# Kernel tuning notes

Hardware: AMD Instinct MI355X
Metric: run time of the kernel (lower is better)

The kernel has to match this reference:

```python
import jax, jax.numpy as jnp
import numpy as np

# Model dims (see init_kwargs)
B, N, N_IN, D = 16, 8192, 4096, 8
DT = 1e-3
TAU_MEM, TAU_ADAPT = 0.02, 0.2
ALPHA = float(np.exp(-DT / TAU_MEM))    # membrane leak decay per step
RHO_A = float(np.exp(-DT / TAU_ADAPT))  # threshold-adaptation decay per step
BETA = 1.8                              # adaptive-threshold strength (ALIF)
TH0 = 1.0                               # base firing threshold
P_SPIKE = 0.05                          # presynaptic firing prob for inputs


def setup_inputs() -> dict:
    key = jax.random.key(0)
    k = jax.random.split(key, 6)
    V = jax.random.normal(k[0], (B, N), jnp.float32)          # membrane potentials
    a = jax.random.uniform(k[1], (B, N), dtype=jnp.float32)   # ALIF adaptation state
    # Delayed-spike ring buffer [D, B, N] and external spikes [B, N_IN] (binary)
    Xd = (jax.random.uniform(k[2], (D, B, N)) < P_SPIKE).astype(jnp.float32)
    Xext = (jax.random.uniform(k[3], (B, N_IN)) < P_SPIKE).astype(jnp.float32)
    # Delta-synapse weights (internal recurrent + one external area)
    W_int = jax.random.normal(k[4], (N, N), jnp.float32) / np.sqrt(N)
    W_ext = jax.random.normal(k[5], (N_IN, N), jnp.float32) / np.sqrt(N_IN)
    return dict(V=V, a=a, Xd=Xd, Xext=Xext, W_int=W_int, W_ext=W_ext)


def reference(V, a, Xd, Xext, W_int, W_ext):
    # --- ALIFSpikes: adaptive threshold spike generation ---
    th = TH0 + BETA * a
    X = (V >= th).astype(V.dtype)            # [B, N] output spikes
    a_new = RHO_A * a + X                    # adaptation integrates spikes
    # --- DeltaSynapse aggregation: internal (delayed) + external currents ---
    current = Xd[-1] @ W_int + Xext @ W_ext  # [B, N]
    # --- Membrane: leaky integrate with reset-on-spike ---
    V_new = ALPHA * V * (1.0 - X) + (1.0 - ALPHA) * current
    # Shift delay buffer (newest spikes enter slot 0)
    Xd_new = jnp.concatenate([X[None], Xd[:-1]], axis=0)
    return X, V_new, a_new, Xd_new
```

## Files before the change

kernel.cpp:

```cpp
#include <hip/hip_runtime.h>
#include <cstdint>
#include <cstddef>

#define NN    8192
#define NIN   4096
#define BB    16
#define BN    131072
#define ROWCH 256
#define NCHI  32
#define NCHE  16
#define NCH   48

static constexpr float ALPHA_F = 0.9512294245007140f;
static constexpr float RHOA_F  = 0.9950124791926823f;
static constexpr float SCALE_F = (float)(1.0 - 0.9512294245007140);

__global__ __launch_bounds__(256) void k_aux(
    const float* __restrict__ Xd, const float* __restrict__ Xext,
    float* __restrict__ out,
    unsigned* __restrict__ mask_int, unsigned* __restrict__ mask_ext)
{
    const int t = blockIdx.x * 256 + threadIdx.x;

    if (t < NN) {
        unsigned m = 0;
        #pragma unroll
        for (int b = 0; b < BB; ++b)
            m |= (Xd[7*BN + b*NN + t] > 0.5f) ? (1u << b) : 0u;
        mask_int[t] = m;
    } else if (t < NN + NIN) {
        const int i = t - NN;
        unsigned m = 0;
        #pragma unroll
        for (int b = 0; b < BB; ++b)
            m |= (Xext[b*NIN + i] > 0.5f) ? (1u << b) : 0u;
        mask_ext[i] = m;
    }

    ((float4*)(out + (size_t)4*BN))[t] = ((const float4*)Xd)[t];
}

__device__ __forceinline__ void accrow(float2 (&acc)[BB], unsigned m, float wx, float wy)
{
    #pragma unroll
    for (int b = 0; b < BB; ++b) {
        const float f = (float)((m >> b) & 1u);
        acc[b].x = __builtin_fmaf(wx, f, acc[b].x);
        acc[b].y = __builtin_fmaf(wy, f, acc[b].y);
    }
}

__global__ __launch_bounds__(256) void k_mm(
    const float* __restrict__ Wint, const float* __restrict__ Wext,
    const unsigned* __restrict__ mask_int, const unsigned* __restrict__ mask_ext,
    float* __restrict__ part)
{
    const int tid  = threadIdx.x;
    const int y    = blockIdx.y;
    const int wave = tid >> 6, lane = tid & 63;
    const bool is_int = (y < NCHI);
    const float*    W    = is_int ? Wint : Wext;
    const unsigned* mask = is_int ? mask_int : mask_ext;
    const int base_row   = (is_int ? y : (y - NCHI)) * ROWCH;

    __shared__ unsigned sc[ROWCH + 16];
    __shared__ unsigned wsum[4];

    const unsigned m = mask[base_row + tid];
    const unsigned long long bal = __ballot(m != 0);
    const unsigned pre = __popcll(bal & ((1ull << lane) - 1ull));
    if (lane == 0) wsum[wave] = (unsigned)__popcll(bal);
    __syncthreads();
    const unsigned w0 = wsum[0], w1 = wsum[1], w2 = wsum[2], w3 = wsum[3];
    unsigned bw = 0;
    if (wave > 0) bw += w0;
    if (wave > 1) bw += w1;
    if (wave > 2) bw += w2;
    const unsigned total = w0 + w1 + w2 + w3;
    if (m) sc[bw + pre] = ((unsigned)tid << 16) | m;
    if (tid < 16) sc[total + tid] = 0u;
    __syncthreads();
    const unsigned nrow8 = (total + 7u) & ~7u;

    const int n = (blockIdx.x << 9) + (tid << 1);
    float2 acc[BB];
    #pragma unroll
    for (int b = 0; b < BB; ++b) acc[b] = make_float2(0.f, 0.f);

    const float* Wb = W + (size_t)base_row * NN + n;

    unsigned eA[8]; float2 wA[8];
    #pragma unroll
    for (int k = 0; k < 8; ++k) eA[k] = sc[k];
    #pragma unroll
    for (int k = 0; k < 8; ++k)
        wA[k] = *(const float2*)(Wb + (int)(eA[k] >> 16) * NN);

    for (unsigned j = 0; j < nrow8; j += 8) {
        unsigned eB[8]; float2 wB[8];
        #pragma unroll
        for (int k = 0; k < 8; ++k) eB[k] = sc[j + 8 + k];
        #pragma unroll
        for (int k = 0; k < 8; ++k)
            wB[k] = *(const float2*)(Wb + (int)(eB[k] >> 16) * NN);
        #pragma unroll
        for (int k = 0; k < 8; ++k)
            accrow(acc, eA[k] & 0xffffu, wA[k].x, wA[k].y);
        #pragma unroll
        for (int k = 0; k < 8; ++k) { eA[k] = eB[k]; wA[k] = wB[k]; }
    }

    float* p = part + (size_t)y * BN + n;
    #pragma unroll
    for (int b = 0; b < BB; ++b)
        *(float2*)(p + (size_t)b * NN) = acc[b];
}

__global__ __launch_bounds__(128) void k_fin(
    const float* __restrict__ V, const float* __restrict__ a,
    const float* __restrict__ part, float* __restrict__ out)
{
    const int t4 = blockIdx.x * 128 + threadIdx.x;

    float4 s = make_float4(0.f, 0.f, 0.f, 0.f);
    #pragma unroll 8
    for (int c = 0; c < NCH; ++c) {
        const float4 p = ((const float4*)(part + (size_t)c * BN))[t4];
        s.x += p.x; s.y += p.y; s.z += p.z; s.w += p.w;
    }

    const float4 v4 = ((const float4*)V)[t4];
    const float4 a4 = ((const float4*)a)[t4];
    float4 x4, vn4, an4;
    {
        const float* vv = &v4.x; const float* aa = &a4.x;
        float* xx = &x4.x; float* vn = &vn4.x; float* an = &an4.x;
        const float* ss = &s.x;
        #pragma unroll
        for (int k = 0; k < 4; ++k) {
            const float th = __fadd_rn(1.0f, __fmul_rn(1.8f, aa[k]));
            const bool spike = (vv[k] >= th);
            const float x = spike ? 1.0f : 0.0f;
            xx[k] = x;
            float v_new = spike ? 0.0f : __fmul_rn(ALPHA_F, vv[k]);
            vn[k] = __builtin_fmaf(SCALE_F, ss[k], v_new);
            an[k] = __fadd_rn(__fmul_rn(RHOA_F, aa[k]), x);
        }
    }
    ((float4*)out)[t4]                       = x4;
    ((float4*)(out + (size_t)BN))[t4]        = vn4;
    ((float4*)(out + (size_t)2*BN))[t4]      = an4;
    ((float4*)(out + (size_t)3*BN))[t4]      = x4;
}

extern "C" void kernel_launch(void* const* d_in, const int* in_sizes, int n_in,
                              void* d_out, int out_size, void* d_ws, size_t ws_size,
                              hipStream_t stream)
{
    const float* V    = (const float*)d_in[0];
    const float* a    = (const float*)d_in[1];
    const float* Xd   = (const float*)d_in[2];
    const float* Xext = (const float*)d_in[3];
    const float* Wint = (const float*)d_in[4];
    const float* Wext = (const float*)d_in[5];
    float* out = (float*)d_out;

    unsigned* mask_int = (unsigned*)d_ws;
    unsigned* mask_ext = mask_int + NN;
    float*    part     = (float*)((char*)d_ws + 65536);

    k_aux<<<(7*BN/4)/256, 256, 0, stream>>>(Xd, Xext, out, mask_int, mask_ext);
    k_mm<<<dim3(16, NCH), 256, 0, stream>>>(Wint, Wext, mask_int, mask_ext, part);
    k_fin<<<BN/4/128, 128, 0, stream>>>(V, a, part, out);
}
```

Measured before the change: 424.1 us.

## Replace per-row mask FMA loop with per-batch spike lists in LDS

Each block now builds, per batch index, a list of active rows in shared memory using LDS atomics, and accumulates W rows only for the batches where they spiked, replacing the old loop that ran 16 masked FMAs for every active row. This cuts VALU work roughly by the spike density, but each row can now be loaded once per batch that spiked instead of once overall (L1/L2 mostly absorbs the repeats). It also adds atomic contention and a fixed list capacity of 64 per batch: a chunk with more than 64 spikes for one batch would overflow the list, and the accumulation order now differs from before.

```diff
diff --git a/kernel.cpp b/kernel.cpp
--- a/kernel.cpp
+++ b/kernel.cpp
@@ -10,6 +10,7 @@
 #define NCHI  32
 #define NCHE  16
 #define NCH   48
+#define LCAP  64
 
 static constexpr float ALPHA_F = 0.9512294245007140f;
 static constexpr float RHOA_F  = 0.9950124791926823f;
@@ -40,74 +41,63 @@
     ((float4*)(out + (size_t)4*BN))[t] = ((const float4*)Xd)[t];
 }
 
-__device__ __forceinline__ void accrow(float2 (&acc)[BB], unsigned m, float wx, float wy)
-{
-    #pragma unroll
-    for (int b = 0; b < BB; ++b) {
-        const float f = (float)((m >> b) & 1u);
-        acc[b].x = __builtin_fmaf(wx, f, acc[b].x);
-        acc[b].y = __builtin_fmaf(wy, f, acc[b].y);
-    }
-}
-
 __global__ __launch_bounds__(256) void k_mm(
     const float* __restrict__ Wint, const float* __restrict__ Wext,
     const unsigned* __restrict__ mask_int, const unsigned* __restrict__ mask_ext,
     float* __restrict__ part)
 {
-    const int tid  = threadIdx.x;
-    const int y    = blockIdx.y;
-    const int wave = tid >> 6, lane = tid & 63;
+    const int tid = threadIdx.x;
+    const int y   = blockIdx.y;
     const bool is_int = (y < NCHI);
     const float*    W    = is_int ? Wint : Wext;
     const unsigned* mask = is_int ? mask_int : mask_ext;
     const int base_row   = (is_int ? y : (y - NCHI)) * ROWCH;
 
-    __shared__ unsigned sc[ROWCH + 16];
-    __shared__ unsigned wsum[4];
+    __shared__ unsigned lst[BB][LCAP];
+    __shared__ unsigned cnt[BB];
 
-    const unsigned m = mask[base_row + tid];
-    const unsigned long long bal = __ballot(m != 0);
-    const unsigned pre = __popcll(bal & ((1ull << lane) - 1ull));
-    if (lane == 0) wsum[wave] = (unsigned)__popcll(bal);
+    if (tid < BB) cnt[tid] = 0u;
     __syncthreads();
-    const unsigned w0 = wsum[0], w1 = wsum[1], w2 = wsum[2], w3 = wsum[3];
-    unsigned bw = 0;
-    if (wave > 0) bw += w0;
-    if (wave > 1) bw += w1;
-    if (wave > 2) bw += w2;
-    const unsigned total = w0 + w1 + w2 + w3;
-    if (m) sc[bw + pre] = ((unsigned)tid << 16) | m;
-    if (tid < 16) sc[total + tid] = 0u;
+
+    unsigned m = mask[base_row + tid];
+    while (m) {
+        const int b = (int)__builtin_ctz(m);
+        m &= m - 1u;
+        const unsigned idx = atomicAdd(&cnt[b], 1u);
+        lst[b][idx] = (unsigned)tid;
+    }
     __syncthreads();
-    const unsigned nrow8 = (total + 7u) & ~7u;
 
     const int n = (blockIdx.x << 9) + (tid << 1);
+    const float* Wb = W + (size_t)base_row * NN + n;
+
     float2 acc[BB];
     #pragma unroll
     for (int b = 0; b < BB; ++b) acc[b] = make_float2(0.f, 0.f);
 
-    const float* Wb = W + (size_t)base_row * NN + n;
-
-    unsigned eA[8]; float2 wA[8];
     #pragma unroll
-    for (int k = 0; k < 8; ++k) eA[k] = sc[k];
-    #pragma unroll
-    for (int k = 0; k < 8; ++k)
-        wA[k] = *(const float2*)(Wb + (int)(eA[k] >> 16) * NN);
-
-    for (unsigned j = 0; j < nrow8; j += 8) {
-        unsigned eB[8]; float2 wB[8];
-        #pragma unroll
-        for (int k = 0; k < 8; ++k) eB[k] = sc[j + 8 + k];
-        #pragma unroll
-        for (int k = 0; k < 8; ++k)
-            wB[k] = *(const float2*)(Wb + (int)(eB[k] >> 16) * NN);
-        #pragma unroll
-        for (int k = 0; k < 8; ++k)
-            accrow(acc, eA[k] & 0xffffu, wA[k].x, wA[k].y);
-        #pragma unroll
-        for (int k = 0; k < 8; ++k) { eA[k] = eB[k]; wA[k] = wB[k]; }
+    for (int b = 0; b < BB; ++b) {
+        const int c = (int)cnt[b];
+        int j = 0;
+        for (; j + 4 <= c; j += 4) {
+            const int r0 = (int)lst[b][j + 0];
+            const int r1 = (int)lst[b][j + 1];
+            const int r2 = (int)lst[b][j + 2];
+            const int r3 = (int)lst[b][j + 3];
+            const float2 w0 = *(const float2*)(Wb + (r0 << 13));
+            const float2 w1 = *(const float2*)(Wb + (r1 << 13));
+            const float2 w2 = *(const float2*)(Wb + (r2 << 13));
+            const float2 w3 = *(const float2*)(Wb + (r3 << 13));
+            acc[b].x += w0.x; acc[b].y += w0.y;
+            acc[b].x += w1.x; acc[b].y += w1.y;
+            acc[b].x += w2.x; acc[b].y += w2.y;
+            acc[b].x += w3.x; acc[b].y += w3.y;
+        }
+        for (; j < c; ++j) {
+            const int r = (int)lst[b][j];
+            const float2 w = *(const float2*)(Wb + (r << 13));
+            acc[b].x += w.x; acc[b].y += w.y;
+        }
     }
 
     float* p = part + (size_t)y * BN + n;
```

Measured after the change: 428.9 us. Within noise of the previous version (+1.1%).
